# Performance work log

Hardware: AMD Instinct MI355X
Metric: run time of the kernel (lower is better)

## Reference

```python
import jax, jax.numpy as jnp
import numpy as np

N_FEAT = 350; D = 512; L = 4; DS = 64; NREG = 6; REG_E = 32
B = 32; S = 2048
CLAMP = 20.0


def _ln(x, g, b, eps=1e-5):
    mu = jnp.mean(x, axis=-1, keepdims=True)
    var = jnp.mean(jnp.square(x - mu), axis=-1, keepdims=True)
    return (x - mu) * jax.lax.rsqrt(var + eps) * g + b


def _slstm(x, ln_g, ln_b, Wi, bi, Wf, bf, Wz, bz, Wo, bo, Wp, bp):
    # x: [B,S,D] -> out: [B,S,D]
    xn = _ln(x, ln_g, ln_b)
    log_i = jnp.clip(jnp.einsum('bsd,de->bse', xn, Wi) + bi, -CLAMP, CLAMP)
    log_f = jnp.clip(jnp.einsum('bsd,de->bse', xn, Wf) + bf, -CLAMP, CLAMP)
    z = jnp.tanh(jnp.einsum('bsd,de->bse', xn, Wz) + bz)
    o = jax.nn.sigmoid(jnp.einsum('bsd,de->bse', xn, Wo) + bo)

    def step(carry, inp):
        m, c = carry
        li, lf, zt, ot = inp
        m_new = jnp.maximum(m + lf, li)
        i_s = jnp.exp(li - m_new)
        f_s = jnp.exp(m + lf - m_new)
        c_new = f_s * c + i_s * zt
        h = ot * jnp.tanh(c_new)
        return (m_new, c_new), h

    bsz = x.shape[0]
    init = (jnp.zeros((bsz, DS), x.dtype), jnp.zeros((bsz, DS), x.dtype))
    seq = (jnp.swapaxes(log_i, 0, 1), jnp.swapaxes(log_f, 0, 1),
           jnp.swapaxes(z, 0, 1), jnp.swapaxes(o, 0, 1))
    _, hs = jax.lax.scan(step, init, seq)  # hs: [S,B,DS]
    hs = jnp.swapaxes(hs, 0, 1)  # [B,S,DS]
    return jnp.einsum('bse,ed->bsd', hs, Wp) + bp


def setup_inputs() -> dict:
    key = jax.random.key(0)
    ks = iter(jax.random.split(key, 64))
    def p(*shape):
        return jax.random.normal(next(ks), shape, dtype=jnp.float32) * 0.02
    return {
        'x': jax.random.normal(next(ks), (B, S, N_FEAT), dtype=jnp.float32),
        'regime_ids': jax.random.randint(next(ks), (B, S), 0, NREG),
        'emb_regime': p(NREG, REG_E),
        'grn_w1': p(N_FEAT + REG_E, D), 'grn_b1': jnp.zeros((D,), jnp.float32),
        'grn_w2': p(D, N_FEAT), 'grn_b2': jnp.zeros((N_FEAT,), jnp.float32),
        'in_w': p(N_FEAT, D), 'in_b': jnp.zeros((D,), jnp.float32),
        'ln_in_g': jnp.ones((L, D), jnp.float32), 'ln_in_b': jnp.zeros((L, D), jnp.float32),
        'wi': p(L, D, DS), 'bi': jnp.zeros((L, DS), jnp.float32),
        'wf': p(L, D, DS), 'bf': jnp.zeros((L, DS), jnp.float32),
        'wz': p(L, D, DS), 'bz': jnp.zeros((L, DS), jnp.float32),
        'wo': p(L, D, DS), 'bo': jnp.zeros((L, DS), jnp.float32),
        'wp': p(L, DS, D), 'bp': jnp.zeros((L, D), jnp.float32),
        'nm_g': jnp.ones((L, D), jnp.float32), 'nm_b': jnp.zeros((L, D), jnp.float32),
        'hd15_w': p(D, 1), 'hd15_b': jnp.zeros((1,), jnp.float32),
        'hd30_w': p(D, 1), 'hd30_b': jnp.zeros((1,), jnp.float32),
        'hv_w': p(D, 3), 'hv_b': jnp.zeros((3,), jnp.float32),
        'hreg_w': p(D, NREG), 'hreg_b': jnp.zeros((NREG,), jnp.float32),
        'hrng_w': p(D, 3), 'hrng_b': jnp.zeros((3,), jnp.float32),
    }


def reference(x, regime_ids, emb_regime, grn_w1, grn_b1, grn_w2, grn_b2,
              in_w, in_b, ln_in_g, ln_in_b, wi, bi, wf, bf, wz, bz, wo, bo,
              wp, bp, nm_g, nm_b, hd15_w, hd15_b, hd30_w, hd30_b,
              hv_w, hv_b, hreg_w, hreg_b, hrng_w, hrng_b):
    # Variable selection network (regime-conditioned feature weights)
    remb = emb_regime[regime_ids]                      # [B,S,32]
    comb = jnp.concatenate([x, remb], axis=-1)         # [B,S,382]
    hidden = jax.nn.elu(jnp.einsum('bsf,fd->bsd', comb, grn_w1) + grn_b1)
    weights = jax.nn.softmax(jnp.einsum('bsd,df->bsf', hidden, grn_w2) + grn_b2, axis=-1)
    xw = x * weights
    h = jnp.einsum('bsf,fd->bsd', xw, in_w) + in_b     # [B,S,D]
    for l in range(L):
        res = _slstm(h, ln_in_g[l], ln_in_b[l], wi[l], bi[l], wf[l], bf[l],
                     wz[l], bz[l], wo[l], bo[l], wp[l], bp[l])
        h = _ln(h + res, nm_g[l], nm_b[l])
    h_last = h[:, -1, :]
    return (jnp.squeeze(h_last @ hd15_w + hd15_b, -1),
            jnp.squeeze(h_last @ hd30_w + hd30_b, -1),
            h_last @ hv_w + hv_b,
            h_last @ hreg_w + hreg_b,
            h_last @ hrng_w + hrng_b,
            h_last,
            weights[:, -1, :])
```

## Files before the change

### kernel.cpp

```cpp
#include <hip/hip_runtime.h>
#include <cmath>

#define NFEAT 350
#define DMODEL 512
#define NLAYER 4
#define DSZ 64
#define REG_E 32
#define BATCH 32
#define SEQ 2048
#define MTOK (BATCH * SEQ)
#define CLAMP_V 20.0f

#define CHUNK 64
#define NCHUNK (SEQ / CHUNK)

typedef short bf16x8 __attribute__((ext_vector_type(8)));
typedef float f32x4 __attribute__((ext_vector_type(4)));

__device__ __forceinline__ unsigned short f2b(float v) {
    union { float f; unsigned int u; } x; x.f = v;
    unsigned int r = x.u + 0x7fffu + ((x.u >> 16) & 1u);
    return (unsigned short)(r >> 16);
}
__device__ __forceinline__ float b2f(unsigned short u) {
    union { unsigned int i; float f; } x; x.i = ((unsigned int)u) << 16;
    return x.f;
}
__device__ __forceinline__ unsigned int pack2(float a, float b) {
    return ((unsigned int)f2b(b) << 16) | f2b(a);
}

__global__ __launch_bounds__(256) void tconv_k(const float* __restrict__ src,
                                               unsigned short* __restrict__ dst,
                                               int K, int N, int Kpad) {
    int k = blockIdx.x * 256 + threadIdx.x;
    int n = blockIdx.y;
    if (k >= Kpad) return;
    float v = (k < K && n < N) ? src[(size_t)k * N + n] : 0.f;
    dst[(size_t)n * Kpad + k] = f2b(v);
}

__global__ __launch_bounds__(256) void tconv_g_k(const float* __restrict__ wi,
                                                 const float* __restrict__ wf,
                                                 const float* __restrict__ wz,
                                                 const float* __restrict__ wo,
                                                 unsigned short* __restrict__ dstH,
                                                 unsigned short* __restrict__ dstL) {
    int k = blockIdx.x * 256 + threadIdx.x;
    int n = blockIdx.y;
    int z = blockIdx.z;
    int l = z >> 2, g = z & 3;
    const float* src = (g == 0 ? wi : g == 1 ? wf : g == 2 ? wz : wo) + (size_t)l * DMODEL * DSZ;
    float v = src[(size_t)k * DSZ + n];
    unsigned short hi = f2b(v);
    unsigned short lo = f2b(v - b2f(hi));
    dstH[(size_t)z * 32768 + (size_t)n * 512 + k] = hi;
    dstL[(size_t)z * 32768 + (size_t)n * 512 + k] = lo;
}

__global__ __launch_bounds__(1024) void gbias_k(const float* bi, const float* bf_,
                                                const float* bz, const float* bo,
                                                float* __restrict__ gbias) {
    int t = threadIdx.x;
    int l = t >> 8, r = t & 255, g = r >> 6, e = r & 63;
    const float* s = (g == 0 ? bi : g == 1 ? bf_ : g == 2 ? bz : bo);
    gbias[t] = s[l * 64 + e];
}

__global__ __launch_bounds__(256) void build_xc_k(const float* __restrict__ x,
                                                  const int* __restrict__ rid,
                                                  const float* __restrict__ emb,
                                                  unsigned short* __restrict__ xc) {
    int i = blockIdx.x * 256 + threadIdx.x;
    int m = i / 192, p = i - m * 192;
    int k = p * 2;
    float a = 0.f, b = 0.f;
    if (k < 350) {
        const float2 v = *(const float2*)(x + (size_t)m * NFEAT + k);
        a = v.x; b = v.y;
    } else if (k < 382) {
        int r = rid[m];
        const float2 v = *(const float2*)(emb + r * REG_E + (k - 350));
        a = v.x; b = v.y;
    }
    ((unsigned int*)xc)[(size_t)m * 192 + p] = pack2(a, b);
}

template <int EPI>
__global__ __launch_bounds__(256) void mgemm_k(const unsigned short* __restrict__ Ab,
                                               const unsigned short* __restrict__ Bt,
                                               const float* __restrict__ bias,
                                               float* __restrict__ Cf,
                                               unsigned short* __restrict__ Cb,
                                               int lda, int ldb, int K, int N, int ldc) {
    __shared__ unsigned short As[128][40];
    __shared__ unsigned short Bs[128][40];
    const int tid = threadIdx.x;
    const int lane = tid & 63;
    const int wave = tid >> 6;
    const int l15 = lane & 15;
    const int quad = lane >> 4;
    const int wm = (wave >> 1) * 64;
    const int wn = (wave & 1) * 64;
    const size_t m0 = (size_t)blockIdx.y * 128;
    const int n0 = blockIdx.x * 128;

    const int sr = tid >> 2;
    const int ku = tid & 3;

    const unsigned short* Br0 = Bt + ((size_t)(n0 + sr)) * ldb + ku * 8;
    const unsigned short* Br1 = Br0 + (size_t)64 * ldb;
    const unsigned short* Ar0 = Ab + (m0 + sr) * (size_t)lda + ku * 8;
    const unsigned short* Ar1 = Ar0 + (size_t)64 * lda;

    f32x4 acc[4][4] = {};

    for (int k0 = 0; k0 < K; k0 += 32) {
        *(uint4*)&As[sr][ku * 8]      = *(const uint4*)(Ar0 + k0);
        *(uint4*)&As[sr + 64][ku * 8] = *(const uint4*)(Ar1 + k0);
        *(uint4*)&Bs[sr][ku * 8]      = *(const uint4*)(Br0 + k0);
        *(uint4*)&Bs[sr + 64][ku * 8] = *(const uint4*)(Br1 + k0);
        __syncthreads();
        bf16x8 af[4], bf[4];
#pragma unroll
        for (int mt = 0; mt < 4; mt++)
            af[mt] = *(const bf16x8*)&As[wm + mt * 16 + l15][quad * 8];
#pragma unroll
        for (int nt = 0; nt < 4; nt++)
            bf[nt] = *(const bf16x8*)&Bs[wn + nt * 16 + l15][quad * 8];
#pragma unroll
        for (int mt = 0; mt < 4; mt++)
#pragma unroll
            for (int nt = 0; nt < 4; nt++)
                acc[mt][nt] = __builtin_amdgcn_mfma_f32_16x16x32_bf16(af[mt], bf[nt], acc[mt][nt], 0, 0, 0);
        __syncthreads();
    }

#pragma unroll
    for (int mt = 0; mt < 4; mt++) {
        int gmb = wm + mt * 16 + quad * 4;
#pragma unroll
        for (int nt = 0; nt < 4; nt++) {
            int gn = n0 + wn + nt * 16 + l15;
            if (gn < N) {
                float bv = bias[gn];
#pragma unroll
                for (int r = 0; r < 4; r++) {
                    size_t gm = m0 + gmb + r;
                    float v = acc[mt][nt][r] + bv;
                    if (EPI == 0) {
                        v = v > 0.f ? v : expm1f(v);
                        Cb[gm * (size_t)ldc + gn] = f2b(v);
                    } else if (EPI == 1) {
                        Cb[gm * (size_t)ldc + gn] = f2b(v);
                    } else {
                        Cf[gm * (size_t)ldc + gn] = v;
                    }
                }
            }
        }
    }
}

__global__ __launch_bounds__(256) void ggemm_k(const float* __restrict__ h,
                                               const unsigned short* __restrict__ BtH,
                                               const unsigned short* __restrict__ BtL,
                                               const float* __restrict__ bias,
                                               const float* __restrict__ mu,
                                               const float* __restrict__ rstd,
                                               const float* __restrict__ lng,
                                               const float* __restrict__ lnb,
                                               float* __restrict__ gates) {
    __shared__ unsigned short AsH[64][40];
    __shared__ unsigned short AsL[64][40];
    __shared__ unsigned short BsH[128][40];
    __shared__ unsigned short BsL[128][40];
    const int tid = threadIdx.x;
    const int lane = tid & 63;
    const int wave = tid >> 6;
    const int l15 = lane & 15;
    const int quad = lane >> 4;
    const int wm = (wave >> 1) * 32;
    const int wn = (wave & 1) * 64;
    const size_t m0 = (size_t)blockIdx.y * 64;
    const int n0 = blockIdx.x * 128;

    const int sr = tid >> 2;
    const int ku = tid & 3;
    const float* Ar = h + (m0 + sr) * (size_t)DMODEL + ku * 8;
    const float muv = mu[m0 + sr];
    const float rsv = rstd[m0 + sr];

    const int br = tid >> 1;
    const int kh = (tid & 1) * 16;
    const unsigned short* BH = BtH + (size_t)(n0 + br) * 512 + kh;
    const unsigned short* BL = BtL + (size_t)(n0 + br) * 512 + kh;

    f32x4 acc[2][4] = {};

    float4 a0_0, a1_0, a0_1, a1_1;
    uint4 vh0_0, vh1_0, vl0_0, vl1_0;
    uint4 vh0_1, vh1_1, vl0_1, vl1_1;

    a0_0 = *(const float4*)(Ar);      a1_0 = *(const float4*)(Ar + 4);
    vh0_0 = *(const uint4*)(BH);      vh1_0 = *(const uint4*)(BH + 8);
    vl0_0 = *(const uint4*)(BL);      vl1_0 = *(const uint4*)(BL + 8);
    a0_1 = *(const float4*)(Ar + 32); a1_1 = *(const float4*)(Ar + 36);
    vh0_1 = *(const uint4*)(BH + 32); vh1_1 = *(const uint4*)(BH + 40);
    vl0_1 = *(const uint4*)(BL + 32); vl1_1 = *(const uint4*)(BL + 40);

    auto stageA = [&](float4 a0, float4 a1, int k0) {
        float4 g0 = *(const float4*)(lng + k0 + ku * 8);
        float4 g1 = *(const float4*)(lng + k0 + ku * 8 + 4);
        float4 c0 = *(const float4*)(lnb + k0 + ku * 8);
        float4 c1 = *(const float4*)(lnb + k0 + ku * 8 + 4);
        float v[8];
        v[0] = (a0.x - muv) * rsv * g0.x + c0.x;
        v[1] = (a0.y - muv) * rsv * g0.y + c0.y;
        v[2] = (a0.z - muv) * rsv * g0.z + c0.z;
        v[3] = (a0.w - muv) * rsv * g0.w + c0.w;
        v[4] = (a1.x - muv) * rsv * g1.x + c1.x;
        v[5] = (a1.y - muv) * rsv * g1.y + c1.y;
        v[6] = (a1.z - muv) * rsv * g1.z + c1.z;
        v[7] = (a1.w - muv) * rsv * g1.w + c1.w;
        unsigned int hw[4], lw[4];
#pragma unroll
        for (int j = 0; j < 4; j++) {
            unsigned short h0 = f2b(v[2 * j]);
            unsigned short h1 = f2b(v[2 * j + 1]);
            unsigned short l0 = f2b(v[2 * j] - b2f(h0));
            unsigned short l1 = f2b(v[2 * j + 1] - b2f(h1));
            hw[j] = (unsigned int)h0 | ((unsigned int)h1 << 16);
            lw[j] = (unsigned int)l0 | ((unsigned int)l1 << 16);
        }
        *(uint4*)&AsH[sr][ku * 8] = *(uint4*)hw;
        *(uint4*)&AsL[sr][ku * 8] = *(uint4*)lw;
    };
    auto stageB = [&](uint4 h0, uint4 h1, uint4 l0, uint4 l1) {
        *(uint4*)&BsH[br][kh]     = h0;
        *(uint4*)&BsH[br][kh + 8] = h1;
        *(uint4*)&BsL[br][kh]     = l0;
        *(uint4*)&BsL[br][kh + 8] = l1;
    };
    auto compute = [&]() {
        bf16x8 ah[2], al[2], bh[4], bl[4];
#pragma unroll
        for (int mt = 0; mt < 2; mt++) {
            ah[mt] = *(const bf16x8*)&AsH[wm + mt * 16 + l15][quad * 8];
            al[mt] = *(const bf16x8*)&AsL[wm + mt * 16 + l15][quad * 8];
        }
#pragma unroll
        for (int nt = 0; nt < 4; nt++) {
            bh[nt] = *(const bf16x8*)&BsH[wn + nt * 16 + l15][quad * 8];
            bl[nt] = *(const bf16x8*)&BsL[wn + nt * 16 + l15][quad * 8];
        }
#pragma unroll
        for (int mt = 0; mt < 2; mt++)
#pragma unroll
            for (int nt = 0; nt < 4; nt++) {
                acc[mt][nt] = __builtin_amdgcn_mfma_f32_16x16x32_bf16(ah[mt], bh[nt], acc[mt][nt], 0, 0, 0);
                acc[mt][nt] = __builtin_amdgcn_mfma_f32_16x16x32_bf16(al[mt], bh[nt], acc[mt][nt], 0, 0, 0);
                acc[mt][nt] = __builtin_amdgcn_mfma_f32_16x16x32_bf16(ah[mt], bl[nt], acc[mt][nt], 0, 0, 0);
            }
    };

    for (int k0 = 0; k0 < DMODEL; k0 += 64) {
        __syncthreads();
        stageA(a0_0, a1_0, k0);
        stageB(vh0_0, vh1_0, vl0_0, vl1_0);
        __syncthreads();
        if (k0 + 64 < DMODEL) {
            a0_0 = *(const float4*)(Ar + k0 + 64);
            a1_0 = *(const float4*)(Ar + k0 + 68);
            vh0_0 = *(const uint4*)(BH + k0 + 64);
            vh1_0 = *(const uint4*)(BH + k0 + 72);
            vl0_0 = *(const uint4*)(BL + k0 + 64);
            vl1_0 = *(const uint4*)(BL + k0 + 72);
        }
        compute();
        __syncthreads();
        stageA(a0_1, a1_1, k0 + 32);
        stageB(vh0_1, vh1_1, vl0_1, vl1_1);
        __syncthreads();
        if (k0 + 96 < DMODEL) {
            a0_1 = *(const float4*)(Ar + k0 + 96);
            a1_1 = *(const float4*)(Ar + k0 + 100);
            vh0_1 = *(const uint4*)(BH + k0 + 96);
            vh1_1 = *(const uint4*)(BH + k0 + 104);
            vl0_1 = *(const uint4*)(BL + k0 + 96);
            vl1_1 = *(const uint4*)(BL + k0 + 104);
        }
        compute();
    }

#pragma unroll
    for (int mt = 0; mt < 2; mt++) {
        int gmb = wm + mt * 16 + quad * 4;
#pragma unroll
        for (int nt = 0; nt < 4; nt++) {
            int gn = n0 + wn + nt * 16 + l15;
            float bv = bias[gn];
            int g = gn >> 6;
#pragma unroll
            for (int r = 0; r < 4; r++) {
                size_t gm = m0 + gmb + r;
                float v = acc[mt][nt][r] + bv;
                if (g < 2) v = fminf(fmaxf(v, -CLAMP_V), CLAMP_V);
                else if (g == 2) v = tanhf(v);
                else v = 1.f / (1.f + expf(-v));
                gates[gm * 256 + gn] = v;
            }
        }
    }
}

__global__ __launch_bounds__(256) void softmax_xw_k(const unsigned short* __restrict__ logits,
                                                    unsigned short* __restrict__ xc,
                                                    float* __restrict__ out_wlast) {
    int tok = blockIdx.x * 4 + (threadIdx.x >> 6);
    int lane = threadIdx.x & 63;
    const unsigned short* lr = logits + (size_t)tok * NFEAT;
    unsigned short* xr = xc + (size_t)tok * 384;
    float v[6];
    float mx = -1e30f;
#pragma unroll
    for (int i = 0; i < 6; i++) {
        int idx = lane + 64 * i;
        v[i] = (idx < NFEAT) ? b2f(lr[idx]) : -1e30f;
        mx = fmaxf(mx, v[i]);
    }
#pragma unroll
    for (int o = 32; o > 0; o >>= 1) mx = fmaxf(mx, __shfl_xor(mx, o, 64));
    float s = 0.f;
#pragma unroll
    for (int i = 0; i < 6; i++) { v[i] = expf(v[i] - mx); s += v[i]; }
#pragma unroll
    for (int o = 32; o > 0; o >>= 1) s += __shfl_xor(s, o, 64);
    float inv = 1.f / s;
    bool last = ((tok & (SEQ - 1)) == SEQ - 1);
    int b = tok >> 11;
#pragma unroll
    for (int i = 0; i < 6; i++) {
        int idx = lane + 64 * i;
        if (idx < NFEAT) {
            float w = v[i] * inv;
            xr[idx] = f2b(w * b2f(xr[idx]));
            if (last) out_wlast[b * NFEAT + idx] = w;
        } else if (idx < 352) {
            xr[idx] = 0;
        }
    }
}

__global__ __launch_bounds__(256) void ln_stats_k(const float* __restrict__ h,
                                                  float* __restrict__ mu,
                                                  float* __restrict__ rstd) {
    int tok = blockIdx.x * 4 + (threadIdx.x >> 6);
    int lane = threadIdx.x & 63;
    const float* row = h + (size_t)tok * DMODEL;
    float s = 0.f, sq = 0.f;
#pragma unroll
    for (int i = 0; i < 8; i++) {
        float v = row[lane + 64 * i];
        s += v;
        sq += v * v;
    }
#pragma unroll
    for (int o = 32; o > 0; o >>= 1) {
        s += __shfl_xor(s, o, 64);
        sq += __shfl_xor(sq, o, 64);
    }
    if (lane == 0) {
        float m = s * (1.f / DMODEL);
        float var = sq * (1.f / DMODEL) - m * m;
        mu[tok] = m;
        rstd[tok] = rsqrtf(var + 1e-5f);
    }
}

__global__ __launch_bounds__(256) void seg_agg_k(const float* __restrict__ gates,
                                                 float* __restrict__ aggF,
                                                 float* __restrict__ aggL,
                                                 float* __restrict__ aggS) {
    int b = blockIdx.x >> 3;
    int cg = blockIdx.x & 7;
    int chunk = cg * 4 + (threadIdx.x >> 6);
    int e = threadIdx.x & 63;
    const float* gp = gates + ((size_t)b * SEQ + (size_t)chunk * CHUNK) * 256;
    float F = 0.f, L = -1e30f, s = 0.f;
#pragma unroll 4
    for (int t = 0; t < CHUNK; t++) {
        const float* q = gp + (size_t)t * 256;
        float li = q[e], lf = q[64 + e], z = q[128 + e];
        float Ln = fmaxf(L + lf, li);
        s = expf(L + lf - Ln) * s + expf(li - Ln) * z;
        L = Ln;
        F += lf;
    }
    int idx = (b * NCHUNK + chunk) * 64 + e;
    aggF[idx] = F; aggL[idx] = L; aggS[idx] = s;
}

__global__ __launch_bounds__(64) void chunk_scan_k(const float* __restrict__ aggF,
                                                   const float* __restrict__ aggL,
                                                   const float* __restrict__ aggS,
                                                   float* __restrict__ stM,
                                                   float* __restrict__ stC) {
    int b = blockIdx.x;
    int e = threadIdx.x;
    float m = 0.f, c = 0.f;
    for (int k = 0; k < NCHUNK; k++) {
        int idx = (b * NCHUNK + k) * 64 + e;
        stM[idx] = m; stC[idx] = c;
        float F = aggF[idx], L = aggL[idx], s = aggS[idx];
        float mn = fmaxf(m + F, L);
        c = expf(m + F - mn) * c + expf(L - mn) * s;
        m = mn;
    }
}

__global__ __launch_bounds__(256) void replay_k(const float* __restrict__ gates,
                                                const float* __restrict__ stM,
                                                const float* __restrict__ stC,
                                                float* __restrict__ hs) {
    int b = blockIdx.x >> 3;
    int cg = blockIdx.x & 7;
    int chunk = cg * 4 + (threadIdx.x >> 6);
    int e = threadIdx.x & 63;
    int s0 = chunk * CHUNK;
    const float* gp = gates + ((size_t)b * SEQ + s0) * 256;
    float* hp = hs + ((size_t)b * SEQ + s0) * DSZ;
    int idx = (b * NCHUNK + chunk) * 64 + e;
    float m = stM[idx], c = stC[idx];
#pragma unroll 4
    for (int t = 0; t < CHUNK; t++) {
        const float* q = gp + (size_t)t * 256;
        float li = q[e], lf = q[64 + e], z = q[128 + e], o = q[192 + e];
        float mlf = m + lf;
        float mn = fmaxf(mlf, li);
        c = expf(mlf - mn) * c + expf(li - mn) * z;
        m = mn;
        hp[(size_t)t * DSZ + e] = o * tanhf(c);
    }
}

__global__ __launch_bounds__(256) void outproj_k(const float* __restrict__ hs,
                                                 const float* __restrict__ wp,
                                                 const float* __restrict__ bp,
                                                 const float* __restrict__ nmg,
                                                 const float* __restrict__ nmb,
                                                 float* __restrict__ h,
                                                 float* __restrict__ mu,
                                                 float* __restrict__ rstd) {
    __shared__ float shs[16][DSZ];
    __shared__ float swp[16][DMODEL];
    int wv = threadIdx.x >> 6;
    int lane = threadIdx.x & 63;
    int tok0 = blockIdx.x * 16;

    {
        const float4* src = (const float4*)(hs + (size_t)tok0 * DSZ);
        ((float4*)&shs[0][0])[threadIdx.x] = src[threadIdx.x];
    }
    __syncthreads();

    float acc[4][8] = {};
    for (int k0 = 0; k0 < DSZ; k0 += 16) {
        const float4* src = (const float4*)(wp + (size_t)k0 * DMODEL);
#pragma unroll
        for (int i = 0; i < 8; i++)
            ((float4*)&swp[0][0])[threadIdx.x + i * 256] = src[threadIdx.x + i * 256];
        __syncthreads();
#pragma unroll
        for (int k = 0; k < 16; k++) {
            float bv[8];
#pragma unroll
            for (int j = 0; j < 8; j++) bv[j] = swp[k][lane + 64 * j];
#pragma unroll
            for (int t = 0; t < 4; t++) {
                float av = shs[wv * 4 + t][k0 + k];
#pragma unroll
                for (int j = 0; j < 8; j++) acc[t][j] += av * bv[j];
            }
        }
        __syncthreads();
    }

#pragma unroll
    for (int t = 0; t < 4; t++) {
        int tok = tok0 + wv * 4 + t;
        float u[8];
        float s = 0.f, sq = 0.f;
#pragma unroll
        for (int j = 0; j < 8; j++) {
            int col = lane + 64 * j;
            float v = h[(size_t)tok * DMODEL + col] + acc[t][j] + bp[col];
            u[j] = v;
            s += v; sq += v * v;
        }
#pragma unroll
        for (int o = 32; o > 0; o >>= 1) { s += __shfl_xor(s, o, 64); sq += __shfl_xor(sq, o, 64); }
        float mean = s * (1.f / DMODEL);
        float var = sq * (1.f / DMODEL) - mean * mean;
        float rs = rsqrtf(var + 1e-5f);
        float s2 = 0.f, sq2 = 0.f;
#pragma unroll
        for (int j = 0; j < 8; j++) {
            int col = lane + 64 * j;
            float v = (u[j] - mean) * rs * nmg[col] + nmb[col];
            h[(size_t)tok * DMODEL + col] = v;
            s2 += v; sq2 += v * v;
        }
#pragma unroll
        for (int o = 32; o > 0; o >>= 1) { s2 += __shfl_xor(s2, o, 64); sq2 += __shfl_xor(sq2, o, 64); }
        if (lane == 0) {
            float m2 = s2 * (1.f / DMODEL);
            float v2 = sq2 * (1.f / DMODEL) - m2 * m2;
            mu[tok] = m2;
            rstd[tok] = rsqrtf(v2 + 1e-5f);
        }
    }
}

__global__ __launch_bounds__(64) void heads_k(const float* __restrict__ h,
                                              const float* hd15_w, const float* hd15_b,
                                              const float* hd30_w, const float* hd30_b,
                                              const float* hv_w, const float* hv_b,
                                              const float* hreg_w, const float* hreg_b,
                                              const float* hrng_w, const float* hrng_b,
                                              float* __restrict__ out) {
    int b = blockIdx.x;
    int lane = threadIdx.x;
    __shared__ float row[DMODEL];
    const float* hp = h + (size_t)(b * SEQ + SEQ - 1) * DMODEL;
#pragma unroll
    for (int i = 0; i < 8; i++) row[lane + 64 * i] = hp[lane + 64 * i];
    __syncthreads();
#pragma unroll
    for (int i = 0; i < 8; i++) out[448 + b * DMODEL + lane + 64 * i] = row[lane + 64 * i];
    if (lane < 14) {
        const float* w; const float* bb;
        int ncol, j, off;
        if (lane == 0)      { w = hd15_w; bb = hd15_b; ncol = 1; j = 0;         off = 0 + b; }
        else if (lane == 1) { w = hd30_w; bb = hd30_b; ncol = 1; j = 0;         off = 32 + b; }
        else if (lane < 5)  { j = lane - 2;  w = hv_w;   bb = hv_b;   ncol = 3; off = 64 + b * 3 + j; }
        else if (lane < 11) { j = lane - 5;  w = hreg_w; bb = hreg_b; ncol = 6; off = 160 + b * 6 + j; }
        else                { j = lane - 11; w = hrng_w; bb = hrng_b; ncol = 3; off = 352 + b * 3 + j; }
        float s = bb[j];
        for (int k = 0; k < DMODEL; k++) s += row[k] * w[k * ncol + j];
        out[off] = s;
    }
}

extern "C" void kernel_launch(void* const* d_in, const int* in_sizes, int n_in,
                              void* d_out, int out_size, void* d_ws, size_t ws_size,
                              hipStream_t stream) {
    (void)in_sizes; (void)n_in; (void)out_size; (void)ws_size;
    const float* x      = (const float*)d_in[0];
    const int*   rid    = (const int*)d_in[1];
    const float* emb    = (const float*)d_in[2];
    const float* grn_w1 = (const float*)d_in[3];
    const float* grn_b1 = (const float*)d_in[4];
    const float* grn_w2 = (const float*)d_in[5];
    const float* grn_b2 = (const float*)d_in[6];
    const float* in_w   = (const float*)d_in[7];
    const float* in_b   = (const float*)d_in[8];
    const float* ln_g   = (const float*)d_in[9];
    const float* ln_b   = (const float*)d_in[10];
    const float* wi     = (const float*)d_in[11];
    const float* bi     = (const float*)d_in[12];
    const float* wf     = (const float*)d_in[13];
    const float* bf_    = (const float*)d_in[14];
    const float* wz     = (const float*)d_in[15];
    const float* bz     = (const float*)d_in[16];
    const float* wo     = (const float*)d_in[17];
    const float* bo     = (const float*)d_in[18];
    const float* wp     = (const float*)d_in[19];
    const float* bp     = (const float*)d_in[20];
    const float* nm_g   = (const float*)d_in[21];
    const float* nm_b   = (const float*)d_in[22];

    float* out = (float*)d_out;
    char* W = (char*)d_ws;

    float* h               = (float*)W;
    unsigned short* hidden = (unsigned short*)W;
    unsigned short* logits = (unsigned short*)(W + 67108864);
    char* RB = W + 134217728;
    unsigned short* xc = (unsigned short*)RB;
    float* gates  = (float*)RB;
    float* hsbuf  = (float*)(RB + 67108864);
    char* RM = W + 218103808;
    float* aggF  = (float*)(RM);
    float* aggL  = (float*)(RM + 262144);
    float* aggS  = (float*)(RM + 524288);
    float* stM   = (float*)(RM + 786432);
    float* stC   = (float*)(RM + 1048576);
    float* mu    = (float*)(RM + 1310720);
    float* rstd  = (float*)(RM + 1572864);
    unsigned short* w1t  = (unsigned short*)(RM + 1835008);
    unsigned short* w2t  = (unsigned short*)(RM + 2228224);
    unsigned short* inwt = (unsigned short*)(RM + 2621440);
    unsigned short* gwtH = (unsigned short*)(RM + 2981888);
    unsigned short* gwtL = (unsigned short*)(RM + 4030464);
    float* gbias         = (float*)(RM + 5079040);

    build_xc_k<<<MTOK * 192 / 256, 256, 0, stream>>>(x, rid, emb, xc);
    tconv_k<<<dim3(2, 512), 256, 0, stream>>>(grn_w1, w1t, 382, 512, 384);
    tconv_k<<<dim3(2, 384), 256, 0, stream>>>(grn_w2, w2t, 512, 350, 512);
    tconv_k<<<dim3(2, 512), 256, 0, stream>>>(in_w, inwt, 350, 512, 352);
    tconv_g_k<<<dim3(2, 64, 16), 256, 0, stream>>>(wi, wf, wz, wo, gwtH, gwtL);
    gbias_k<<<1, 1024, 0, stream>>>(bi, bf_, bz, bo, gbias);

    mgemm_k<0><<<dim3(4, 512), 256, 0, stream>>>(xc, w1t, grn_b1, nullptr, hidden,
                                                 384, 384, 384, 512, 512);
    mgemm_k<1><<<dim3(3, 512), 256, 0, stream>>>(hidden, w2t, grn_b2, nullptr, logits,
                                                 512, 512, 512, 350, 350);
    softmax_xw_k<<<MTOK / 4, 256, 0, stream>>>(logits, xc, out + 16832);
    mgemm_k<3><<<dim3(4, 512), 256, 0, stream>>>(xc, inwt, in_b, h, nullptr,
                                                 384, 352, 352, 512, 512);
    ln_stats_k<<<MTOK / 4, 256, 0, stream>>>(h, mu, rstd);

    for (int l = 0; l < NLAYER; l++) {
        ggemm_k<<<dim3(2, 1024), 256, 0, stream>>>(h,
                                                   gwtH + (size_t)l * 131072,
                                                   gwtL + (size_t)l * 131072,
                                                   gbias + l * 256,
                                                   mu, rstd,
                                                   ln_g + l * DMODEL, ln_b + l * DMODEL,
                                                   gates);
        seg_agg_k<<<BATCH * 8, 256, 0, stream>>>(gates, aggF, aggL, aggS);
        chunk_scan_k<<<BATCH, 64, 0, stream>>>(aggF, aggL, aggS, stM, stC);
        replay_k<<<BATCH * 8, 256, 0, stream>>>(gates, stM, stC, hsbuf);

        outproj_k<<<MTOK / 16, 256, 0, stream>>>(hsbuf,
                                                 wp + (size_t)l * DSZ * DMODEL,
                                                 bp + l * DMODEL,
                                                 nm_g + l * DMODEL,
                                                 nm_b + l * DMODEL,
                                                 h, mu, rstd);
    }

    heads_k<<<BATCH, 64, 0, stream>>>(h,
                                      (const float*)d_in[23], (const float*)d_in[24],
                                      (const float*)d_in[25], (const float*)d_in[26],
                                      (const float*)d_in[27], (const float*)d_in[28],
                                      (const float*)d_in[29], (const float*)d_in[30],
                                      (const float*)d_in[31], (const float*)d_in[32],
                                      out);
}
```

Measured before the change: 1.497 ms.

## Fuse LN stats into GEMM epilogues, inline chunk scan, widen outproj tiles

Removes the separate ln_stats pass by accumulating row sums and squared sums in the input-projection GEMM epilogue with atomics, and has outproj store raw sums instead of mu/rstd. The gate GEMM now derives mean and rstd from these sums itself. The chunk_scan kernel is dropped: each replay thread recomputes its prefix state serially from the chunk aggregates. Outproj processes 32 tokens per block instead of 16, and gate stores become nontemporal. The changes cut kernel launches and a full read of h, at the cost of redundant prefix work, atomics, and extra register pressure in outproj.

```diff
diff --git a/kernel.cpp b/kernel.cpp
--- a/kernel.cpp
+++ b/kernel.cpp
@@ -28,6 +28,10 @@
 }
 __device__ __forceinline__ unsigned int pack2(float a, float b) {
     return ((unsigned int)f2b(b) << 16) | f2b(a);
+}
+
+__global__ __launch_bounds__(256) void zero_k(float* __restrict__ p) {
+    p[blockIdx.x * 256 + threadIdx.x] = 0.f;
 }
 
 __global__ __launch_bounds__(256) void tconv_k(const float* __restrict__ src,
@@ -92,6 +96,8 @@
                                                const float* __restrict__ bias,
                                                float* __restrict__ Cf,
                                                unsigned short* __restrict__ Cb,
+                                               float* __restrict__ statS,
+                                               float* __restrict__ statQ,
                                                int lda, int ldb, int K, int N, int ldc) {
     __shared__ unsigned short As[128][40];
     __shared__ unsigned short Bs[128][40];
@@ -139,6 +145,8 @@
 #pragma unroll
     for (int mt = 0; mt < 4; mt++) {
         int gmb = wm + mt * 16 + quad * 4;
+        float srow[4] = {0.f, 0.f, 0.f, 0.f};
+        float sqrow[4] = {0.f, 0.f, 0.f, 0.f};
 #pragma unroll
         for (int nt = 0; nt < 4; nt++) {
             int gn = n0 + wn + nt * 16 + l15;
@@ -155,7 +163,24 @@
                         Cb[gm * (size_t)ldc + gn] = f2b(v);
                     } else {
                         Cf[gm * (size_t)ldc + gn] = v;
+                        srow[r] += v;
+                        sqrow[r] += v * v;
                     }
+                }
+            }
+        }
+        if (EPI == 3) {
+#pragma unroll
+            for (int r = 0; r < 4; r++) {
+                float s = srow[r], q = sqrow[r];
+#pragma unroll
+                for (int o = 1; o < 16; o <<= 1) {
+                    s += __shfl_xor(s, o, 64);
+                    q += __shfl_xor(q, o, 64);
+                }
+                if (l15 == 0) {
+                    atomicAdd(&statS[m0 + gmb + r], s);
+                    atomicAdd(&statQ[m0 + gmb + r], q);
                 }
             }
         }
@@ -166,8 +191,8 @@
                                                const unsigned short* __restrict__ BtH,
                                                const unsigned short* __restrict__ BtL,
                                                const float* __restrict__ bias,
-                                               const float* __restrict__ mu,
-                                               const float* __restrict__ rstd,
+                                               const float* __restrict__ statS,
+                                               const float* __restrict__ statQ,
                                                const float* __restrict__ lng,
                                                const float* __restrict__ lnb,
                                                float* __restrict__ gates) {
@@ -188,8 +213,10 @@
     const int sr = tid >> 2;
     const int ku = tid & 3;
     const float* Ar = h + (m0 + sr) * (size_t)DMODEL + ku * 8;
-    const float muv = mu[m0 + sr];
-    const float rsv = rstd[m0 + sr];
+    const float sS = statS[m0 + sr];
+    const float sQ = statQ[m0 + sr];
+    const float muv = sS * (1.f / DMODEL);
+    const float rsv = rsqrtf(sQ * (1.f / DMODEL) - muv * muv + 1e-5f);
 
     const int br = tid >> 1;
     const int kh = (tid & 1) * 16;
@@ -308,7 +335,7 @@
                 if (g < 2) v = fminf(fmaxf(v, -CLAMP_V), CLAMP_V);
                 else if (g == 2) v = tanhf(v);
                 else v = 1.f / (1.f + expf(-v));
-                gates[gm * 256 + gn] = v;
+                __builtin_nontemporal_store(v, &gates[gm * 256 + gn]);
             }
         }
     }
@@ -349,32 +376,6 @@
         } else if (idx < 352) {
             xr[idx] = 0;
         }
-    }
-}
-
-__global__ __launch_bounds__(256) void ln_stats_k(const float* __restrict__ h,
-                                                  float* __restrict__ mu,
-                                                  float* __restrict__ rstd) {
-    int tok = blockIdx.x * 4 + (threadIdx.x >> 6);
-    int lane = threadIdx.x & 63;
-    const float* row = h + (size_t)tok * DMODEL;
-    float s = 0.f, sq = 0.f;
-#pragma unroll
-    for (int i = 0; i < 8; i++) {
-        float v = row[lane + 64 * i];
-        s += v;
-        sq += v * v;
-    }
-#pragma unroll
-    for (int o = 32; o > 0; o >>= 1) {
-        s += __shfl_xor(s, o, 64);
-        sq += __shfl_xor(sq, o, 64);
-    }
-    if (lane == 0) {
-        float m = s * (1.f / DMODEL);
-        float var = sq * (1.f / DMODEL) - m * m;
-        mu[tok] = m;
-        rstd[tok] = rsqrtf(var + 1e-5f);
     }
 }
 
@@ -401,37 +402,28 @@
     aggF[idx] = F; aggL[idx] = L; aggS[idx] = s;
 }
 
-__global__ __launch_bounds__(64) void chunk_scan_k(const float* __restrict__ aggF,
-                                                   const float* __restrict__ aggL,
-                                                   const float* __restrict__ aggS,
-                                                   float* __restrict__ stM,
-                                                   float* __restrict__ stC) {
-    int b = blockIdx.x;
-    int e = threadIdx.x;
-    float m = 0.f, c = 0.f;
-    for (int k = 0; k < NCHUNK; k++) {
-        int idx = (b * NCHUNK + k) * 64 + e;
-        stM[idx] = m; stC[idx] = c;
-        float F = aggF[idx], L = aggL[idx], s = aggS[idx];
-        float mn = fmaxf(m + F, L);
-        c = expf(m + F - mn) * c + expf(L - mn) * s;
-        m = mn;
-    }
-}
-
 __global__ __launch_bounds__(256) void replay_k(const float* __restrict__ gates,
-                                                const float* __restrict__ stM,
-                                                const float* __restrict__ stC,
+                                                const float* __restrict__ aggF,
+                                                const float* __restrict__ aggL,
+                                                const float* __restrict__ aggS,
                                                 float* __restrict__ hs) {
     int b = blockIdx.x >> 3;
     int cg = blockIdx.x & 7;
     int chunk = cg * 4 + (threadIdx.x >> 6);
     int e = threadIdx.x & 63;
+
+    float m = 0.f, c = 0.f;
+    for (int k = 0; k < chunk; k++) {
+        int idx = (b * NCHUNK + k) * 64 + e;
+        float F = aggF[idx], L = aggL[idx], s = aggS[idx];
+        float mn = fmaxf(m + F, L);
+        c = expf(m + F - mn) * c + expf(L - mn) * s;
+        m = mn;
+    }
+
     int s0 = chunk * CHUNK;
     const float* gp = gates + ((size_t)b * SEQ + s0) * 256;
     float* hp = hs + ((size_t)b * SEQ + s0) * DSZ;
-    int idx = (b * NCHUNK + chunk) * 64 + e;
-    float m = stM[idx], c = stC[idx];
 #pragma unroll 4
     for (int t = 0; t < CHUNK; t++) {
         const float* q = gp + (size_t)t * 256;
@@ -450,26 +442,28 @@
                                                  const float* __restrict__ nmg,
                                                  const float* __restrict__ nmb,
                                                  float* __restrict__ h,
-                                                 float* __restrict__ mu,
-                                                 float* __restrict__ rstd) {
-    __shared__ float shs[16][DSZ];
+                                                 float* __restrict__ statS,
+                                                 float* __restrict__ statQ) {
+    __shared__ float shs[32][DSZ];
     __shared__ float swp[16][DMODEL];
-    int wv = threadIdx.x >> 6;
-    int lane = threadIdx.x & 63;
-    int tok0 = blockIdx.x * 16;
+    int tid = threadIdx.x;
+    int wv = tid >> 6;
+    int lane = tid & 63;
+    int tok0 = blockIdx.x * 32;
 
     {
         const float4* src = (const float4*)(hs + (size_t)tok0 * DSZ);
-        ((float4*)&shs[0][0])[threadIdx.x] = src[threadIdx.x];
+        ((float4*)&shs[0][0])[tid]       = src[tid];
+        ((float4*)&shs[0][0])[tid + 256] = src[tid + 256];
     }
     __syncthreads();
 
-    float acc[4][8] = {};
+    float acc[8][8] = {};
     for (int k0 = 0; k0 < DSZ; k0 += 16) {
         const float4* src = (const float4*)(wp + (size_t)k0 * DMODEL);
 #pragma unroll
         for (int i = 0; i < 8; i++)
-            ((float4*)&swp[0][0])[threadIdx.x + i * 256] = src[threadIdx.x + i * 256];
+            ((float4*)&swp[0][0])[tid + i * 256] = src[tid + i * 256];
         __syncthreads();
 #pragma unroll
         for (int k = 0; k < 16; k++) {
@@ -477,8 +471,8 @@
 #pragma unroll
             for (int j = 0; j < 8; j++) bv[j] = swp[k][lane + 64 * j];
 #pragma unroll
-            for (int t = 0; t < 4; t++) {
-                float av = shs[wv * 4 + t][k0 + k];
+            for (int t = 0; t < 8; t++) {
+                float av = shs[wv * 8 + t][k0 + k];
 #pragma unroll
                 for (int j = 0; j < 8; j++) acc[t][j] += av * bv[j];
             }
@@ -487,8 +481,8 @@
     }
 
 #pragma unroll
-    for (int t = 0; t < 4; t++) {
-        int tok = tok0 + wv * 4 + t;
+    for (int t = 0; t < 8; t++) {
+        int tok = tok0 + wv * 8 + t;
         float u[8];
         float s = 0.f, sq = 0.f;
 #pragma unroll
@@ -514,10 +508,8 @@
 #pragma unroll
         for (int o = 32; o > 0; o >>= 1) { s2 += __shfl_xor(s2, o, 64); sq2 += __shfl_xor(sq2, o, 64); }
         if (lane == 0) {
-            float m2 = s2 * (1.f / DMODEL);
-            float v2 = sq2 * (1.f / DMODEL) - m2 * m2;
-            mu[tok] = m2;
-            rstd[tok] = rsqrtf(v2 + 1e-5f);
+            statS[tok] = s2;
+            statQ[tok] = sq2;
         }
     }
 }
@@ -594,10 +586,8 @@
     float* aggF  = (float*)(RM);
     float* aggL  = (float*)(RM + 262144);
     float* aggS  = (float*)(RM + 524288);
-    float* stM   = (float*)(RM + 786432);
-    float* stC   = (float*)(RM + 1048576);
-    float* mu    = (float*)(RM + 1310720);
-    float* rstd  = (float*)(RM + 1572864);
+    float* statS = (float*)(RM + 1310720);
+    float* statQ = (float*)(RM + 1572864);
     unsigned short* w1t  = (unsigned short*)(RM + 1835008);
     unsigned short* w2t  = (unsigned short*)(RM + 2228224);
     unsigned short* inwt = (unsigned short*)(RM + 2621440);
@@ -606,6 +596,7 @@
     float* gbias         = (float*)(RM + 5079040);
 
     build_xc_k<<<MTOK * 192 / 256, 256, 0, stream>>>(x, rid, emb, xc);
+    zero_k<<<512, 256, 0, stream>>>(statS);
     tconv_k<<<dim3(2, 512), 256, 0, stream>>>(grn_w1, w1t, 382, 512, 384);
     tconv_k<<<dim3(2, 384), 256, 0, stream>>>(grn_w2, w2t, 512, 350, 512);
     tconv_k<<<dim3(2, 512), 256, 0, stream>>>(in_w, inwt, 350, 512, 352);
@@ -613,32 +604,30 @@
     gbias_k<<<1, 1024, 0, stream>>>(bi, bf_, bz, bo, gbias);
 
     mgemm_k<0><<<dim3(4, 512), 256, 0, stream>>>(xc, w1t, grn_b1, nullptr, hidden,
-                                                 384, 384, 384, 512, 512);
+                                                 nullptr, nullptr, 384, 384, 384, 512, 512);
     mgemm_k<1><<<dim3(3, 512), 256, 0, stream>>>(hidden, w2t, grn_b2, nullptr, logits,
-                                                 512, 512, 512, 350, 350);
+                                                 nullptr, nullptr, 512, 512, 512, 350, 350);
     softmax_xw_k<<<MTOK / 4, 256, 0, stream>>>(logits, xc, out + 16832);
     mgemm_k<3><<<dim3(4, 512), 256, 0, stream>>>(xc, inwt, in_b, h, nullptr,
-                                                 384, 352, 352, 512, 512);
-    ln_stats_k<<<MTOK / 4, 256, 0, stream>>>(h, mu, rstd);
+                                                 statS, statQ, 384, 352, 352, 512, 512);
 
     for (int l = 0; l < NLAYER; l++) {
         ggemm_k<<<dim3(2, 1024), 256, 0, stream>>>(h,
                                                    gwtH + (size_t)l * 131072,
                                                    gwtL + (size_t)l * 131072,
                                                    gbias + l * 256,
-                                                   mu, rstd,
+                                                   statS, statQ,
                                                    ln_g + l * DMODEL, ln_b + l * DMODEL,
                                                    gates);
         seg_agg_k<<<BATCH * 8, 256, 0, stream>>>(gates, aggF, aggL, aggS);
-        chunk_scan_k<<<BATCH, 64, 0, stream>>>(aggF, aggL, aggS, stM, stC);
-        replay_k<<<BATCH * 8, 256, 0, stream>>>(gates, stM, stC, hsbuf);
-
-        outproj_k<<<MTOK / 16, 256, 0, stream>>>(hsbuf,
+        replay_k<<<BATCH * 8, 256, 0, stream>>>(gates, aggF, aggL, aggS, hsbuf);
+
+        outproj_k<<<MTOK / 32, 256, 0, stream>>>(hsbuf,
                                                  wp + (size_t)l * DSZ * DMODEL,
                                                  bp + l * DMODEL,
                                                  nm_g + l * DMODEL,
                                                  nm_b + l * DMODEL,
-                                                 h, mu, rstd);
+                                                 h, statS, statQ);
     }
 
     heads_k<<<BATCH, 64, 0, stream>>>(h,
```

New measurement: 1.595 ms. +6.6%, slower.
